# Kernel tuning notes

Measured on AMD Instinct MI355X. Metric: run time of the kernel, lower is better.

## Reference

```python
import jax, jax.numpy as jnp
import numpy as np

SPATIAL = 8  # spatial_size


def setup_inputs() -> dict:
    key = jax.random.key(0)
    k1, k2 = jax.random.split(key)
    B, C, T, H, W = 8, 1, 16, 500, 500
    inp = jax.random.normal(k1, (B, C, T, H, W), dtype=jnp.float32)
    stdv = 1.0 / np.sqrt(T)  # matches reset_parameters scaling
    weight = jax.random.uniform(k2, (T, 4, 4), dtype=jnp.float32, minval=-stdv, maxval=stdv)
    return {"input": inp, "weight": weight, "pad_h": 512, "pad_w": 512,
            "n_patch_h": 127, "n_patch_w": 127}


def reference(input, weight, pad_h, pad_w, n_patch_h, n_patch_w):
    B, C, T, H, W = input.shape
    step = weight.shape[1]  # spatial_size // 2 (overlapping)
    s = SPATIAL

    # zero-pad bottom/right to the padded frame size
    x = jnp.pad(input, ((0, 0), (0, 0), (0, 0), (0, pad_h - H), (0, pad_w - W)))

    # weight.repeat(B, C, 1, n_patch_h+1, n_patch_w+1): tile step-blocks over frame;
    # broadcast over (B, C) instead of materializing the full repeat.
    w_tiled = jnp.tile(weight, (1, n_patch_h + 1, n_patch_w + 1))  # (T, pad_h, pad_w)

    # masked multiply + temporal sum -> coded snapshot (B, C, pad_h, pad_w)
    output = jnp.einsum('bcthw,thw->bchw', x, w_tiled)

    # overlapping patch extraction: unfold(2, s, step).unfold(3, s, step)
    hh = (jnp.arange(n_patch_h) * step)[:, None] + jnp.arange(s)  # (nph, s)
    ww = (jnp.arange(n_patch_w) * step)[:, None] + jnp.arange(s)  # (npw, s)
    patches = output[:, :, hh[:, None, :, None], ww[None, :, None, :]]  # (B,C,nph,npw,s,s)

    # permute(0,1,2,3,5,4) then flatten to (B, C*nph*npw, s*s)
    patches = jnp.swapaxes(patches, -1, -2)
    patches = patches.reshape(B, -1, s * s)

    return patches, output[:, :, :H, :W]
```

## Files before the change

kernel.cpp:

```cpp
#include <hip/hip_runtime.h>

#define B_DIM 8
#define T_DIM 16
#define H_IN 500
#define W_IN 500
#define NPH 127
#define NPW 127
#define STEP 4
#define LSTR 516

typedef float f4 __attribute__((ext_vector_type(4)));

__global__ __launch_bounds__(256) void k_band(const float* __restrict__ in,
                                              const float* __restrict__ wgt,
                                              float* __restrict__ patches,
                                              float* __restrict__ crop) {
    __shared__ float lds[8 * LSTR];
    __shared__ f4 wlds[T_DIM * 4];
    int tid = threadIdx.x;
    if (tid < T_DIM * 4) wlds[tid] = reinterpret_cast<const f4*>(wgt)[tid];

    int orig = blockIdx.x;
    int n = (orig & 7) * 64 + (orig >> 3);
    int q = n & 63;
    int b = n >> 6;
    __syncthreads();

    #pragma unroll
    for (int k = 0; k < 4; ++k) {
        int e = tid + k * 256;
        int r = e >> 7;
        int c = (e & 127) * 4;
        int h = q * 8 + r;
        f4 acc = {0.f, 0.f, 0.f, 0.f};
        if (h < H_IN && c < W_IN) {
            const float* base = in + (size_t)b * T_DIM * (H_IN * W_IN) + h * W_IN + c;
            int hr = h & 3;
            #pragma unroll
            for (int t = 0; t < T_DIM; ++t) {
                f4 xv = __builtin_nontemporal_load(
                    reinterpret_cast<const f4*>(base + (size_t)t * (H_IN * W_IN)));
                acc += xv * wlds[t * 4 + hr];
            }
            *reinterpret_cast<f4*>(crop + ((size_t)b * H_IN + h) * W_IN + c) = acc;
        }
        *reinterpret_cast<f4*>(&lds[r * LSTR + c]) = acc;
    }
    __syncthreads();

    {
        f4* dst = reinterpret_cast<f4*>(patches + (((size_t)b * NPH + 2 * q) * NPW) * 64);
        for (int e4 = tid; e4 < NPW * 16; e4 += 256) {
            int i0 = (e4 & 1) * 4;
            int j  = (e4 >> 1) & 7;
            int pw = e4 >> 4;
            int col = pw * STEP + j;
            f4 v;
            v.x = lds[(i0 + 0) * LSTR + col];
            v.y = lds[(i0 + 1) * LSTR + col];
            v.z = lds[(i0 + 2) * LSTR + col];
            v.w = lds[(i0 + 3) * LSTR + col];
            dst[e4] = v;
        }
    }
    if (q < 63) {
        f4* dst = reinterpret_cast<f4*>(patches + (((size_t)b * NPH + 2 * q + 1) * NPW) * 64);
        for (int e = tid; e < NPW * 8; e += 256) {
            int j  = e & 7;
            int pw = e >> 3;
            int col = pw * STEP + j;
            f4 v;
            v.x = lds[4 * LSTR + col];
            v.y = lds[5 * LSTR + col];
            v.z = lds[6 * LSTR + col];
            v.w = lds[7 * LSTR + col];
            dst[pw * 16 + j * 2] = v;
        }
    }
    if (q > 0) {
        f4* dst = reinterpret_cast<f4*>(patches + (((size_t)b * NPH + 2 * q - 1) * NPW) * 64);
        for (int e = tid; e < NPW * 8; e += 256) {
            int j  = e & 7;
            int pw = e >> 3;
            int col = pw * STEP + j;
            f4 v;
            v.x = lds[0 * LSTR + col];
            v.y = lds[1 * LSTR + col];
            v.z = lds[2 * LSTR + col];
            v.w = lds[3 * LSTR + col];
            dst[pw * 16 + j * 2 + 1] = v;
        }
    }
}

extern "C" void kernel_launch(void* const* d_in, const int* in_sizes, int n_in,
                              void* d_out, int out_size, void* d_ws, size_t ws_size,
                              hipStream_t stream) {
    const float* in  = (const float*)d_in[0];
    const float* wgt = (const float*)d_in[1];
    float* out     = (float*)d_out;
    float* patches = out;
    float* crop    = out + (size_t)B_DIM * NPH * NPW * 64;

    k_band<<<B_DIM * 64, 256, 0, stream>>>(in, wgt, patches, crop);
}
```

Before: 35.74 us.

## Use 16-row bands with inter-block flag handoff for boundary rows

Blocks now cover 16-row bands with 512 threads, so 256 blocks replace 512, and each block writes full patch rows instead of half-rows scattered across neighbours. The four boundary rows needed from the next band are published to a workspace buffer and signalled with a flag. The consumer spins on that flag with a bounded wait and falls back to recomputing the rows if the wait times out. Non-temporal loads are replaced by plain loads. This adds a memset launch, workspace traffic and a spin dependency between blocks, which could serialize if the producer block is not resident.

```diff
diff --git a/kernel.cpp b/kernel.cpp
--- a/kernel.cpp
+++ b/kernel.cpp
@@ -6,89 +6,125 @@
 #define W_IN 500
 #define NPH 127
 #define NPW 127
-#define STEP 4
 #define LSTR 516
+#define NT 512
+#define BANDS 32
+#define ROWS 16
+#define MAXSPIN 65536
 
 typedef float f4 __attribute__((ext_vector_type(4)));
 
-__global__ __launch_bounds__(256) void k_band(const float* __restrict__ in,
-                                              const float* __restrict__ wgt,
-                                              float* __restrict__ patches,
-                                              float* __restrict__ crop) {
-    __shared__ float lds[8 * LSTR];
+__global__ __launch_bounds__(NT) void k_band(const float* __restrict__ in,
+                                             const float* __restrict__ wgt,
+                                             float* __restrict__ patches,
+                                             float* __restrict__ crop,
+                                             int* __restrict__ flags,
+                                             float* __restrict__ bnd,
+                                             int use_ws) {
+    __shared__ float lds[(ROWS + 4) * LSTR];
     __shared__ f4 wlds[T_DIM * 4];
+    __shared__ int s_ready;
     int tid = threadIdx.x;
     if (tid < T_DIM * 4) wlds[tid] = reinterpret_cast<const f4*>(wgt)[tid];
 
     int orig = blockIdx.x;
-    int n = (orig & 7) * 64 + (orig >> 3);
-    int q = n & 63;
-    int b = n >> 6;
+    int b = orig & 7;
+    int q = orig >> 3;
     __syncthreads();
 
     #pragma unroll
     for (int k = 0; k < 4; ++k) {
-        int e = tid + k * 256;
+        int e = tid + k * NT;
         int r = e >> 7;
         int c = (e & 127) * 4;
-        int h = q * 8 + r;
+        int h = q * ROWS + r;
         f4 acc = {0.f, 0.f, 0.f, 0.f};
         if (h < H_IN && c < W_IN) {
             const float* base = in + (size_t)b * T_DIM * (H_IN * W_IN) + h * W_IN + c;
             int hr = h & 3;
             #pragma unroll
-            for (int t = 0; t < T_DIM; ++t) {
-                f4 xv = __builtin_nontemporal_load(
-                    reinterpret_cast<const f4*>(base + (size_t)t * (H_IN * W_IN)));
-                acc += xv * wlds[t * 4 + hr];
-            }
+            for (int t = 0; t < T_DIM; ++t)
+                acc += *reinterpret_cast<const f4*>(base + (size_t)t * (H_IN * W_IN))
+                       * wlds[t * 4 + hr];
             *reinterpret_cast<f4*>(crop + ((size_t)b * H_IN + h) * W_IN + c) = acc;
         }
         *reinterpret_cast<f4*>(&lds[r * LSTR + c]) = acc;
+        if (k == 0 && use_ws) {
+            *reinterpret_cast<f4*>(bnd + (size_t)(b * BANDS + q) * 2048 + r * 512 + c) = acc;
+        }
     }
     __syncthreads();
+    if (use_ws && tid == 0) {
+        __threadfence();
+        atomicExch(&flags[b * BANDS + q], 1);
+    }
 
-    {
-        f4* dst = reinterpret_cast<f4*>(patches + (((size_t)b * NPH + 2 * q) * NPW) * 64);
-        for (int e4 = tid; e4 < NPW * 16; e4 += 256) {
+    f4* pbase = reinterpret_cast<f4*>(patches)
+              + ((size_t)b * NPH + (size_t)4 * q) * NPW * 16;
+    for (int sub = 0; sub < 3; ++sub) {
+        f4* dst = pbase + (size_t)sub * NPW * 16;
+        for (int e4 = tid; e4 < NPW * 16; e4 += NT) {
             int i0 = (e4 & 1) * 4;
             int j  = (e4 >> 1) & 7;
             int pw = e4 >> 4;
-            int col = pw * STEP + j;
+            int col = pw * 4 + j;
+            int r0 = sub * 4 + i0;
             f4 v;
-            v.x = lds[(i0 + 0) * LSTR + col];
-            v.y = lds[(i0 + 1) * LSTR + col];
-            v.z = lds[(i0 + 2) * LSTR + col];
-            v.w = lds[(i0 + 3) * LSTR + col];
+            v.x = lds[(r0 + 0) * LSTR + col];
+            v.y = lds[(r0 + 1) * LSTR + col];
+            v.z = lds[(r0 + 2) * LSTR + col];
+            v.w = lds[(r0 + 3) * LSTR + col];
             dst[e4] = v;
         }
     }
-    if (q < 63) {
-        f4* dst = reinterpret_cast<f4*>(patches + (((size_t)b * NPH + 2 * q + 1) * NPW) * 64);
-        for (int e = tid; e < NPW * 8; e += 256) {
-            int j  = e & 7;
-            int pw = e >> 3;
-            int col = pw * STEP + j;
+
+    if (q < BANDS - 1) {
+        if (tid == 0) {
+            int ok = 0;
+            if (use_ws) {
+                for (int it = 0; it < MAXSPIN; ++it) {
+                    if (atomicAdd(&flags[b * BANDS + q + 1], 0) == 1) { ok = 1; break; }
+                    __builtin_amdgcn_s_sleep(8);
+                }
+                if (ok) __threadfence();
+            }
+            s_ready = ok;
+        }
+        __syncthreads();
+        {
+            int r = tid >> 7;
+            int c = (tid & 127) * 4;
+            if (s_ready) {
+                *reinterpret_cast<f4*>(&lds[(ROWS + r) * LSTR + c]) =
+                    *reinterpret_cast<const f4*>(bnd + (size_t)(b * BANDS + q + 1) * 2048 + r * 512 + c);
+            } else {
+                int h = (q + 1) * ROWS + r;
+                f4 acc = {0.f, 0.f, 0.f, 0.f};
+                if (h < H_IN && c < W_IN) {
+                    const float* base = in + (size_t)b * T_DIM * (H_IN * W_IN) + h * W_IN + c;
+                    int hr = h & 3;
+                    #pragma unroll
+                    for (int t = 0; t < T_DIM; ++t)
+                        acc += *reinterpret_cast<const f4*>(base + (size_t)t * (H_IN * W_IN))
+                               * wlds[t * 4 + hr];
+                }
+                *reinterpret_cast<f4*>(&lds[(ROWS + r) * LSTR + c]) = acc;
+            }
+        }
+        __syncthreads();
+        f4* dst = pbase + (size_t)3 * NPW * 16;
+        for (int e4 = tid; e4 < NPW * 16; e4 += NT) {
+            int i0 = (e4 & 1) * 4;
+            int j  = (e4 >> 1) & 7;
+            int pw = e4 >> 4;
+            int col = pw * 4 + j;
+            int r0 = 12 + i0;
             f4 v;
-            v.x = lds[4 * LSTR + col];
-            v.y = lds[5 * LSTR + col];
-            v.z = lds[6 * LSTR + col];
-            v.w = lds[7 * LSTR + col];
-            dst[pw * 16 + j * 2] = v;
-        }
-    }
-    if (q > 0) {
-        f4* dst = reinterpret_cast<f4*>(patches + (((size_t)b * NPH + 2 * q - 1) * NPW) * 64);
-        for (int e = tid; e < NPW * 8; e += 256) {
-            int j  = e & 7;
-            int pw = e >> 3;
-            int col = pw * STEP + j;
-            f4 v;
-            v.x = lds[0 * LSTR + col];
-            v.y = lds[1 * LSTR + col];
-            v.z = lds[2 * LSTR + col];
-            v.w = lds[3 * LSTR + col];
-            dst[pw * 16 + j * 2 + 1] = v;
+            v.x = lds[(r0 + 0) * LSTR + col];
+            v.y = lds[(r0 + 1) * LSTR + col];
+            v.z = lds[(r0 + 2) * LSTR + col];
+            v.w = lds[(r0 + 3) * LSTR + col];
+            dst[e4] = v;
         }
     }
 }
@@ -102,5 +138,11 @@
     float* patches = out;
     float* crop    = out + (size_t)B_DIM * NPH * NPW * 64;
 
-    k_band<<<B_DIM * 64, 256, 0, stream>>>(in, wgt, patches, crop);
+    size_t need = 256 * sizeof(int) + (size_t)256 * 2048 * sizeof(float);
+    int use_ws = (ws_size >= need) ? 1 : 0;
+    int*   flags = (int*)d_ws;
+    float* bnd   = (float*)d_ws + 256;
+
+    if (use_ws) hipMemsetAsync(flags, 0, 256 * sizeof(int), stream);
+    k_band<<<B_DIM * BANDS, NT, 0, stream>>>(in, wgt, patches, crop, flags, bnd, use_ws);
 }
```

After: 52.36 us. 46.5% more time.
